# Kernel tuning notes

Measured on AMD Instinct MI355X. Metric: run time of the kernel, lower is better.

The kernel has to match this reference:

```python
import jax, jax.numpy as jnp
import numpy as np

N_QUBITS = 16
DEPTH = 4
BATCH = 512
DIM = 2 ** N_QUBITS


def _rot_matrix(tx, ty, tz):
    """Combined U = RZ(tz) @ RY(ty) @ RX(tx) per batch element. t* : [B] -> U : [B,2,2] complex64."""
    cx = jnp.cos(tx / 2).astype(jnp.complex64); sx = jnp.sin(tx / 2).astype(jnp.complex64)
    cy = jnp.cos(ty / 2).astype(jnp.complex64); sy = jnp.sin(ty / 2).astype(jnp.complex64)
    ez = jnp.exp(-1j * (tz / 2).astype(jnp.complex64))
    RX = jnp.stack([jnp.stack([cx, -1j * sx], -1), jnp.stack([-1j * sx, cx], -1)], -2)
    RY = jnp.stack([jnp.stack([cy, -sy], -1), jnp.stack([sy, cy], -1)], -2)
    zr = jnp.zeros_like(ez)
    RZ = jnp.stack([jnp.stack([ez, zr], -1), jnp.stack([zr, jnp.conj(ez)], -1)], -2)
    return jnp.einsum('bij,bjk,bkl->bil', RZ, RY, RX)


def _apply_1q(state, U, q):
    """Apply per-sample 2x2 gate U [B,2,2] on wire q (wire 0 = most significant bit)."""
    B = state.shape[0]
    st = state.reshape(B, 2 ** q, 2, 2 ** (N_QUBITS - 1 - q))
    st = jnp.einsum('bij,bajc->baic', U, st)
    return st.reshape(B, DIM)


def _apply_cnot(state, c, t):
    """CNOT with control wire c, target wire t."""
    B = state.shape[0]
    st = state.reshape((B,) + (2,) * N_QUBITS)
    ctrl0 = jax.lax.index_in_dim(st, 0, axis=1 + c, keepdims=True)
    ctrl1 = jnp.flip(jax.lax.index_in_dim(st, 1, axis=1 + c, keepdims=True), axis=1 + t)
    st = jnp.concatenate([ctrl0, ctrl1], axis=1 + c)
    return st.reshape(B, DIM)


def setup_inputs() -> dict:
    key = jax.random.key(0)
    k1, k2 = jax.random.split(key)
    x = jax.random.normal(k1, (BATCH, N_QUBITS), dtype=jnp.float32)
    params = jax.random.normal(k2, (DEPTH, N_QUBITS, 3), dtype=jnp.float32)
    return {"x": x, "params": params}


def reference(x, params):
    angles = jnp.tanh(x)  # [B, n_qubits]
    B = angles.shape[0]
    state = jnp.zeros((B, DIM), dtype=jnp.complex64).at[:, 0].set(1.0)
    for d in range(DEPTH):
        for q in range(N_QUBITS):
            a = angles[:, q]
            U = _rot_matrix(a + params[d, q, 0], a + params[d, q, 1], a + params[d, q, 2])
            state = _apply_1q(state, U, q)
        for q in range(N_QUBITS - 1):
            state = _apply_cnot(state, q, q + 1)
        state = _apply_cnot(N_QUBITS - 1 and state or state, N_QUBITS - 1, 0) if False else _apply_cnot(state, N_QUBITS - 1, 0)
    probs = (state.real ** 2 + state.imag ** 2)  # [B, DIM]
    zs = []
    for q in range(N_QUBITS):
        p = probs.reshape(B, 2 ** q, 2, 2 ** (N_QUBITS - 1 - q))
        zs.append((p[:, :, 0, :] - p[:, :, 1, :]).sum(axis=(1, 2)))
    return jnp.stack(zs, axis=1)  # [B, n_qubits]
```

## Files before the change

### kernel.cpp

```cpp
#include <hip/hip_runtime.h>
#include <cstdint>
#include <utility>

#define NQ 16
#define NDEPTH 4
#define NBATCH 512
#define NTHR 512
#define NAMP 128
#define NREG 93
#define NLDS (NAMP - NREG)

typedef float vf2 __attribute__((ext_vector_type(2)));
typedef float vf4 __attribute__((ext_vector_type(4)));

struct Masks {
  unsigned short delta[NDEPTH][NQ];
  unsigned short rowm[NDEPTH][NQ];
  unsigned short meas[NQ];
};

constexpr Masks make_masks() {
  Masks m = {};
  unsigned short Arow[NQ] = {};
  unsigned short Ainv[NQ] = {};
  for (int p = 0; p < NQ; ++p) {
    Arow[p] = (unsigned short)(1u << p);
    Ainv[p] = (unsigned short)(1u << p);
  }
  for (int d = 0; d < NDEPTH; ++d) {
    for (int q = 0; q < NQ; ++q) {
      m.delta[d][q] = Ainv[15 - q];
      m.rowm[d][q]  = Arow[15 - q];
    }
    for (int q = 0; q < NQ - 1; ++q) {
      const int pc = 15 - q, pt = 15 - (q + 1);
      Arow[pt] = (unsigned short)(Arow[pt] ^ Arow[pc]);
      Ainv[pc] = (unsigned short)(Ainv[pc] ^ Ainv[pt]);
    }
    {
      const int pc = 0, pt = 15;
      Arow[pt] = (unsigned short)(Arow[pt] ^ Arow[pc]);
      Ainv[pc] = (unsigned short)(Ainv[pc] ^ Ainv[pt]);
    }
  }
  for (int q = 0; q < NQ; ++q) m.meas[q] = Arow[15 - q];
  return m;
}

constexpr Masks MK = make_masks();

constexpr int cpar(int v) {
  int p = 0;
  for (int i = 0; i < 16; ++i) p ^= (v >> i) & 1;
  return p;
}

template<typename F, int... Is>
__device__ __forceinline__ void sf_impl(F&& f, std::integer_sequence<int, Is...>) {
  (f(std::integral_constant<int, Is>{}), ...);
}
template<int N, typename F>
__device__ __forceinline__ void static_for(F&& f) {
  sf_impl(f, std::make_integer_sequence<int, N>{});
}

__device__ __forceinline__ vf2 swap2(vf2 v) {
  return __builtin_shufflevector(v, v, 1, 0);
}
__device__ __forceinline__ vf2 upd(vf2 Arr, vf2 Ain, vf2 Brr, vf2 Bin,
                                   vf2 m, vf2 p) {
  vf2 t = Arr * m;
  t = __builtin_elementwise_fma(Ain, swap2(m), t);
  t = __builtin_elementwise_fma(Brr, p, t);
  t = __builtin_elementwise_fma(Bin, swap2(p), t);
  return t;
}

template<int r>
__device__ __forceinline__ vf2 getamp(const vf2 (&s)[NREG], const vf2* sst, int tid) {
  if constexpr (r < NREG) return s[r];
  else return sst[(r - NREG) * NTHR + tid];
}
template<int r>
__device__ __forceinline__ void putamp(vf2 (&s)[NREG], vf2* sst, int tid, vf2 v) {
  if constexpr (r < NREG) s[r] = v;
  else sst[(r - NREG) * NTHR + tid] = v;
}

template<int D, int Q>
__device__ __forceinline__ void apply_gate(vf2 (&s)[NREG], vf2* sst, vf4* xch,
                                           const vf4* utab, int tid) {
  constexpr int DLT   = MK.delta[D][Q];
  constexpr int R     = MK.rowm[D][Q];
  constexpr int dreg  = DLT & (NAMP - 1);
  constexpr int dthr  = DLT >> 7;
  constexpr int dlane = dthr & 63;
  constexpr int dwave = dthr >> 6;

  const int pt = __popc(tid & (R >> 7)) & 1;
  const int gbase = (D * NQ + Q) * 4;
  const int o0 = pt << 1;
  const int o1 = 2 - o0;
  const vf4 ca0 = utab[gbase + o0], cb0 = utab[gbase + o0 + 1];
  const vf4 ca1 = utab[gbase + o1], cb1 = utab[gbase + o1 + 1];
  const vf2 A0rr = {ca0.x, ca0.y}, A0in = {ca0.z, ca0.w};
  const vf2 B0rr = {cb0.x, cb0.y}, B0in = {cb0.z, cb0.w};
  const vf2 A1rr = {ca1.x, ca1.y}, A1in = {ca1.z, ca1.w};
  const vf2 B1rr = {cb1.x, cb1.y}, B1in = {cb1.z, cb1.w};

  if constexpr (dthr == 0) {
    static_for<NAMP>([&](auto rc) {
      constexpr int r = decltype(rc)::value;
      constexpr int r2 = r ^ dreg;
      if constexpr (r < r2) {
        constexpr int p0 = cpar(r & R);
        constexpr int p1 = cpar(r2 & R);
        const vf2 a = getamp<r >(s, sst, tid);
        const vf2 c = getamp<r2>(s, sst, tid);
        const vf2 n0 = p0 ? upd(A1rr, A1in, B1rr, B1in, a, c)
                           : upd(A0rr, A0in, B0rr, B0in, a, c);
        const vf2 n1 = p1 ? upd(A1rr, A1in, B1rr, B1in, c, a)
                           : upd(A0rr, A0in, B0rr, B0in, c, a);
        putamp<r >(s, sst, tid, n0);
        putamp<r2>(s, sst, tid, n1);
      }
    });
  } else if constexpr (dwave == 0) {
    if constexpr (dreg == 0) {
      static_for<4>([&](auto bc) {
        constexpr int BB = decltype(bc)::value;
        static_for<32>([&](auto jc) {
          constexpr int r = 32 * BB + decltype(jc)::value;
          constexpr int p0 = cpar(r & R);
          const vf2 m = getamp<r>(s, sst, tid);
          vf2 p;
          p.x = __shfl_xor(m.x, dlane);
          p.y = __shfl_xor(m.y, dlane);
          const vf2 n = p0 ? upd(A1rr, A1in, B1rr, B1in, m, p)
                            : upd(A0rr, A0in, B0rr, B0in, m, p);
          putamp<r>(s, sst, tid, n);
        });
        __builtin_amdgcn_sched_barrier(0);
      });
    } else {
      static_for<4>([&](auto bc) {
        constexpr int BB = decltype(bc)::value;
        static_for<32>([&](auto jc) {
          constexpr int r = 32 * BB + decltype(jc)::value;
          constexpr int r2 = r ^ dreg;
          if constexpr (r < r2) {
            constexpr int p0 = cpar(r & R);
            constexpr int p1 = cpar(r2 & R);
            const vf2 m0 = getamp<r >(s, sst, tid);
            const vf2 m1 = getamp<r2>(s, sst, tid);
            vf2 p0v, p1v;
            p0v.x = __shfl_xor(m1.x, dlane);
            p0v.y = __shfl_xor(m1.y, dlane);
            p1v.x = __shfl_xor(m0.x, dlane);
            p1v.y = __shfl_xor(m0.y, dlane);
            const vf2 n0 = p0 ? upd(A1rr, A1in, B1rr, B1in, m0, p0v)
                               : upd(A0rr, A0in, B0rr, B0in, m0, p0v);
            const vf2 n1 = p1 ? upd(A1rr, A1in, B1rr, B1in, m1, p1v)
                               : upd(A0rr, A0in, B0rr, B0in, m1, p1v);
            putamp<r >(s, sst, tid, n0);
            putamp<r2>(s, sst, tid, n1);
          }
        });
        __builtin_amdgcn_sched_barrier(0);
      });
    }
  } else {
    const int ptid = tid ^ dthr;
    if constexpr (dreg < 4) {
      static_for<NAMP / 4>([&](auto kc) {
        constexpr int k = decltype(kc)::value;
        const vf2 m0 = getamp<4 * k + 0>(s, sst, tid);
        const vf2 m1 = getamp<4 * k + 1>(s, sst, tid);
        const vf2 m2 = getamp<4 * k + 2>(s, sst, tid);
        const vf2 m3 = getamp<4 * k + 3>(s, sst, tid);
        xch[tid]        = (vf4){m0.x, m0.y, m1.x, m1.y};
        xch[NTHR + tid] = (vf4){m2.x, m2.y, m3.x, m3.y};
        __syncthreads();
        const vf4 q0 = xch[ptid];
        const vf4 q1 = xch[NTHR + ptid];
        static_for<4>([&](auto jc) {
          constexpr int j = decltype(jc)::value;
          constexpr int r = 4 * k + j;
          constexpr int jp = j ^ dreg;
          constexpr int p0 = cpar(r & R);
          const vf2 m = (j == 0) ? m0 : (j == 1) ? m1 : (j == 2) ? m2 : m3;
          vf2 p;
          if constexpr (jp == 0)      p = (vf2){q0.x, q0.y};
          else if constexpr (jp == 1) p = (vf2){q0.z, q0.w};
          else if constexpr (jp == 2) p = (vf2){q1.x, q1.y};
          else                        p = (vf2){q1.z, q1.w};
          const vf2 n = p0 ? upd(A1rr, A1in, B1rr, B1in, m, p)
                            : upd(A0rr, A0in, B0rr, B0in, m, p);
          putamp<r>(s, sst, tid, n);
        });
        __syncthreads();
      });
    } else {
      constexpr int kx = dreg >> 2;
      constexpr int dj = dreg & 3;
      static_for<NAMP / 4>([&](auto cc) {
        constexpr int c = decltype(cc)::value;
        if constexpr (c < (c ^ kx)) {
          constexpr int c2 = c ^ kx;
          {
            const vf2 a0 = getamp<4 * c + 0>(s, sst, tid);
            const vf2 a1 = getamp<4 * c + 1>(s, sst, tid);
            const vf2 a2 = getamp<4 * c + 2>(s, sst, tid);
            const vf2 a3 = getamp<4 * c + 3>(s, sst, tid);
            xch[tid]        = (vf4){a0.x, a0.y, a1.x, a1.y};
            xch[NTHR + tid] = (vf4){a2.x, a2.y, a3.x, a3.y};
          }
          __syncthreads();
          vf2 t0, t1, t2, t3;
          {
            const vf4 q0 = xch[ptid];
            const vf4 q1 = xch[NTHR + ptid];
            static_for<4>([&](auto jc) {
              constexpr int j = decltype(jc)::value;
              constexpr int r = 4 * c2 + j;
              constexpr int jp = j ^ dj;
              constexpr int p0 = cpar(r & R);
              const vf2 m = getamp<r>(s, sst, tid);
              vf2 p;
              if constexpr (jp == 0)      p = (vf2){q0.x, q0.y};
              else if constexpr (jp == 1) p = (vf2){q0.z, q0.w};
              else if constexpr (jp == 2) p = (vf2){q1.x, q1.y};
              else                        p = (vf2){q1.z, q1.w};
              const vf2 n = p0 ? upd(A1rr, A1in, B1rr, B1in, m, p)
                                : upd(A0rr, A0in, B0rr, B0in, m, p);
              if constexpr (j == 0) t0 = n;
              else if constexpr (j == 1) t1 = n;
              else if constexpr (j == 2) t2 = n;
              else t3 = n;
            });
          }
          __syncthreads();
          {
            const vf2 a0 = getamp<4 * c2 + 0>(s, sst, tid);
            const vf2 a1 = getamp<4 * c2 + 1>(s, sst, tid);
            const vf2 a2 = getamp<4 * c2 + 2>(s, sst, tid);
            const vf2 a3 = getamp<4 * c2 + 3>(s, sst, tid);
            xch[tid]        = (vf4){a0.x, a0.y, a1.x, a1.y};
            xch[NTHR + tid] = (vf4){a2.x, a2.y, a3.x, a3.y};
          }
          __syncthreads();
          {
            const vf4 q0 = xch[ptid];
            const vf4 q1 = xch[NTHR + ptid];
            static_for<4>([&](auto jc) {
              constexpr int j = decltype(jc)::value;
              constexpr int r = 4 * c + j;
              constexpr int jp = j ^ dj;
              constexpr int p0 = cpar(r & R);
              const vf2 m = getamp<r>(s, sst, tid);
              vf2 p;
              if constexpr (jp == 0)      p = (vf2){q0.x, q0.y};
              else if constexpr (jp == 1) p = (vf2){q0.z, q0.w};
              else if constexpr (jp == 2) p = (vf2){q1.x, q1.y};
              else                        p = (vf2){q1.z, q1.w};
              const vf2 n = p0 ? upd(A1rr, A1in, B1rr, B1in, m, p)
                                : upd(A0rr, A0in, B0rr, B0in, m, p);
              putamp<r>(s, sst, tid, n);
            });
          }
          putamp<4 * c2 + 0>(s, sst, tid, t0);
          putamp<4 * c2 + 1>(s, sst, tid, t1);
          putamp<4 * c2 + 2>(s, sst, tid, t2);
          putamp<4 * c2 + 3>(s, sst, tid, t3);
          __syncthreads();
        }
      });
    }
  }
}

template<int D, int Q>
__device__ __forceinline__ void apply_all(vf2 (&s)[NREG], vf2* sst, vf4* xch,
                                          const vf4* utab, int tid) {
  apply_gate<D, Q>(s, sst, xch, utab, tid);
  __builtin_amdgcn_sched_barrier(0);
  if constexpr (Q < NQ - 1) {
    apply_all<D, Q + 1>(s, sst, xch, utab, tid);
  } else if constexpr (D < NDEPTH - 1) {
    apply_all<D + 1, 0>(s, sst, xch, utab, tid);
  }
}

__global__ __launch_bounds__(NTHR)
__attribute__((amdgpu_waves_per_eu(2, 2)))
void qsim_kernel(const float* __restrict__ x,
                 const float* __restrict__ params,
                 float* __restrict__ out) {
  __shared__ vf2 sst[NLDS * NTHR];
  __shared__ vf4 xch[2 * NTHR];
  __shared__ vf4 utab[NDEPTH * NQ * 4];

  const int tid = threadIdx.x;
  const int b = blockIdx.x;

  if (tid < NDEPTH * NQ) {
    const int d = tid / NQ, q = tid % NQ;
    const float a = tanhf(x[b * NQ + q]);
    const float tx = a + params[(d * NQ + q) * 3 + 0];
    const float ty = a + params[(d * NQ + q) * 3 + 1];
    const float tz = a + params[(d * NQ + q) * 3 + 2];
    const float cx = cosf(0.5f * tx), sx = sinf(0.5f * tx);
    const float cy = cosf(0.5f * ty), sy = sinf(0.5f * ty);
    const float cz = cosf(0.5f * tz), sz = sinf(0.5f * tz);
    const float m00r = cy * cx,  m00i =  sy * sx;
    const float m01r = -sy * cx, m01i = -cy * sx;
    const float m10r = sy * cx,  m10i = -cy * sx;
    const float m11r = cy * cx,  m11i = -sy * sx;
    const float u00r = cz * m00r + sz * m00i, u00i = cz * m00i - sz * m00r;
    const float u01r = cz * m01r + sz * m01i, u01i = cz * m01i - sz * m01r;
    const float u10r = cz * m10r - sz * m10i, u10i = cz * m10i + sz * m10r;
    const float u11r = cz * m11r - sz * m11i, u11i = cz * m11i + sz * m11r;
    vf4* slot = utab + tid * 4;
    slot[0] = (vf4){u00r, u00r, -u00i, u00i};
    slot[1] = (vf4){u01r, u01r, -u01i, u01i};
    slot[2] = (vf4){u11r, u11r, -u11i, u11i};
    slot[3] = (vf4){u10r, u10r, -u10i, u10i};
  }

  vf2 s[NREG];
  static_for<NREG>([&](auto rc) { s[decltype(rc)::value] = (vf2){0.f, 0.f}; });
  static_for<NLDS>([&](auto ic) {
    sst[decltype(ic)::value * NTHR + tid] = (vf2){0.f, 0.f};
  });
  if (tid == 0) s[0].x = 1.0f;
  __syncthreads();

  apply_all<0, 0>(s, sst, xch, utab, tid);

  __syncthreads();
  float* red = (float*)xch;
  static_for<2>([&](auto hc) {
    constexpr int H = decltype(hc)::value;
    float z[8];
    static_for<8>([&](auto qc) { z[decltype(qc)::value] = 0.f; });
    static_for<NAMP>([&](auto rc) {
      constexpr int r = decltype(rc)::value;
      const vf2 v = getamp<r>(s, sst, tid);
      const float pr = v.x * v.x + v.y * v.y;
      static_for<8>([&](auto qc) {
        constexpr int qq = decltype(qc)::value;
        constexpr int q = 8 * H + qq;
        constexpr bool neg = cpar(r & MK.meas[q]) != 0;
        z[qq] = neg ? (z[qq] - pr) : (z[qq] + pr);
      });
    });
    static_for<8>([&](auto qc) {
      constexpr int qq = decltype(qc)::value;
      constexpr int q = 8 * H + qq;
      const int ptq = __popc(tid & (MK.meas[q] >> 7)) & 1;
      float v = ptq ? -z[qq] : z[qq];
      static_for<6>([&](auto ic) {
        constexpr int sh = 32 >> decltype(ic)::value;
        v += __shfl_xor(v, sh);
      });
      z[qq] = v;
    });
    if ((tid & 63) == 0) {
      const int w = tid >> 6;
      static_for<8>([&](auto qc) {
        constexpr int qq = decltype(qc)::value;
        red[w * 8 + qq] = z[qq];
      });
    }
    __syncthreads();
    if (tid < 8) {
      float acc = 0.f;
#pragma unroll
      for (int w = 0; w < 8; ++w) acc += red[w * 8 + tid];
      out[b * NQ + 8 * H + tid] = acc;
    }
    __syncthreads();
  });
}

extern "C" void kernel_launch(void* const* d_in, const int* in_sizes, int n_in,
                              void* d_out, int out_size, void* d_ws, size_t ws_size,
                              hipStream_t stream) {
  const float* x      = (const float*)d_in[0];
  const float* params = (const float*)d_in[1];
  float* out          = (float*)d_out;
  qsim_kernel<<<dim3(NBATCH), dim3(NTHR), 0, stream>>>(x, params, out);
}
```

Measured before the change: 854.3 us.

## Use DPP for small lane swaps and halve barriers in cross-wave gate exchange

Cross-lane exchanges with XOR distances 1, 2, 3, 7 and 15 now use DPP update instructions instead of ds_bpermute-based shuffles. The cross-wave exchange path is unified: each round stages two 4-amplitude groups (8 amplitudes) through a larger LDS buffer and uses one barrier pair per 8 amplitudes, instead of two or four barriers per group. The register-resident amplitude count rises from 93 to 97 to cut LDS-resident state. Risks include register pressure or spills at the fixed two waves per EU, and the doubled exchange buffer raising LDS use.

```diff
diff --git a/kernel.cpp b/kernel.cpp
--- a/kernel.cpp
+++ b/kernel.cpp
@@ -7,7 +7,7 @@
 #define NBATCH 512
 #define NTHR 512
 #define NAMP 128
-#define NREG 93
+#define NREG 97
 #define NLDS (NAMP - NREG)
 
 typedef float vf2 __attribute__((ext_vector_type(2)));
@@ -55,6 +55,11 @@
   return p;
 }
 
+constexpr int dppctrl(int dl) {
+  return dl == 1 ? 0xB1 : dl == 2 ? 0x4E : dl == 3 ? 0x1B
+       : dl == 7 ? 0x141 : dl == 15 ? 0x140 : -1;
+}
+
 template<typename F, int... Is>
 __device__ __forceinline__ void sf_impl(F&& f, std::integer_sequence<int, Is...>) {
   (f(std::integral_constant<int, Is>{}), ...);
@@ -76,6 +81,22 @@
   return t;
 }
 
+template<int DL>
+__device__ __forceinline__ vf2 xlane(vf2 v) {
+  constexpr int C = dppctrl(DL);
+  if constexpr (C >= 0) {
+    int xi = __float_as_int(v.x), yi = __float_as_int(v.y);
+    xi = __builtin_amdgcn_update_dpp(xi, xi, C, 0xF, 0xF, true);
+    yi = __builtin_amdgcn_update_dpp(yi, yi, C, 0xF, 0xF, true);
+    return (vf2){__int_as_float(xi), __int_as_float(yi)};
+  } else {
+    vf2 p;
+    p.x = __shfl_xor(v.x, DL);
+    p.y = __shfl_xor(v.y, DL);
+    return p;
+  }
+}
+
 template<int r>
 __device__ __forceinline__ vf2 getamp(const vf2 (&s)[NREG], const vf2* sst, int tid) {
   if constexpr (r < NREG) return s[r];
@@ -85,6 +106,12 @@
 __device__ __forceinline__ void putamp(vf2 (&s)[NREG], vf2* sst, int tid, vf2 v) {
   if constexpr (r < NREG) s[r] = v;
   else sst[(r - NREG) * NTHR + tid] = v;
+}
+template<int r>
+__device__ __forceinline__ vf4 pack2(const vf2 (&s)[NREG], const vf2* sst, int tid) {
+  const vf2 a = getamp<r    >(s, sst, tid);
+  const vf2 b = getamp<r + 1>(s, sst, tid);
+  return (vf4){a.x, a.y, b.x, b.y};
 }
 
 template<int D, int Q>
@@ -133,9 +160,7 @@
           constexpr int r = 32 * BB + decltype(jc)::value;
           constexpr int p0 = cpar(r & R);
           const vf2 m = getamp<r>(s, sst, tid);
-          vf2 p;
-          p.x = __shfl_xor(m.x, dlane);
-          p.y = __shfl_xor(m.y, dlane);
+          const vf2 p = xlane<dlane>(m);
           const vf2 n = p0 ? upd(A1rr, A1in, B1rr, B1in, m, p)
                             : upd(A0rr, A0in, B0rr, B0in, m, p);
           putamp<r>(s, sst, tid, n);
@@ -153,11 +178,8 @@
             constexpr int p1 = cpar(r2 & R);
             const vf2 m0 = getamp<r >(s, sst, tid);
             const vf2 m1 = getamp<r2>(s, sst, tid);
-            vf2 p0v, p1v;
-            p0v.x = __shfl_xor(m1.x, dlane);
-            p0v.y = __shfl_xor(m1.y, dlane);
-            p1v.x = __shfl_xor(m0.x, dlane);
-            p1v.y = __shfl_xor(m0.y, dlane);
+            const vf2 p0v = xlane<dlane>(m1);
+            const vf2 p1v = xlane<dlane>(m0);
             const vf2 n0 = p0 ? upd(A1rr, A1in, B1rr, B1in, m0, p0v)
                                : upd(A0rr, A0in, B0rr, B0in, m0, p0v);
             const vf2 n1 = p1 ? upd(A1rr, A1in, B1rr, B1in, m1, p1v)
@@ -170,112 +192,43 @@
       });
     }
   } else {
+    constexpr int kc0 = dreg >> 2;
+    constexpr int kc  = kc0 ? kc0 : 1;
     const int ptid = tid ^ dthr;
-    if constexpr (dreg < 4) {
-      static_for<NAMP / 4>([&](auto kc) {
-        constexpr int k = decltype(kc)::value;
-        const vf2 m0 = getamp<4 * k + 0>(s, sst, tid);
-        const vf2 m1 = getamp<4 * k + 1>(s, sst, tid);
-        const vf2 m2 = getamp<4 * k + 2>(s, sst, tid);
-        const vf2 m3 = getamp<4 * k + 3>(s, sst, tid);
-        xch[tid]        = (vf4){m0.x, m0.y, m1.x, m1.y};
-        xch[NTHR + tid] = (vf4){m2.x, m2.y, m3.x, m3.y};
+    static_for<NAMP / 4>([&](auto cc) {
+      constexpr int c = decltype(cc)::value;
+      if constexpr (c < (c ^ kc)) {
+        constexpr int c2 = c ^ kc;
+        xch[0 * NTHR + tid] = pack2<4 * c  + 0>(s, sst, tid);
+        xch[1 * NTHR + tid] = pack2<4 * c  + 2>(s, sst, tid);
+        xch[2 * NTHR + tid] = pack2<4 * c2 + 0>(s, sst, tid);
+        xch[3 * NTHR + tid] = pack2<4 * c2 + 2>(s, sst, tid);
         __syncthreads();
-        const vf4 q0 = xch[ptid];
-        const vf4 q1 = xch[NTHR + ptid];
-        static_for<4>([&](auto jc) {
-          constexpr int j = decltype(jc)::value;
-          constexpr int r = 4 * k + j;
-          constexpr int jp = j ^ dreg;
+        const vf4 q0 = xch[0 * NTHR + ptid];
+        const vf4 q1 = xch[1 * NTHR + ptid];
+        const vf4 q2 = xch[2 * NTHR + ptid];
+        const vf4 q3 = xch[3 * NTHR + ptid];
+        static_for<8>([&](auto jc) {
+          constexpr int jj = decltype(jc)::value;
+          constexpr int r  = (jj < 4) ? (4 * c + jj) : (4 * c2 + (jj - 4));
+          constexpr int rp = r ^ dreg;
+          constexpr int sb = ((rp >> 2) == c) ? 0 : 2;
+          constexpr int slot = sb + ((rp & 3) >> 1);
+          constexpr int half = rp & 1;
           constexpr int p0 = cpar(r & R);
-          const vf2 m = (j == 0) ? m0 : (j == 1) ? m1 : (j == 2) ? m2 : m3;
           vf2 p;
-          if constexpr (jp == 0)      p = (vf2){q0.x, q0.y};
-          else if constexpr (jp == 1) p = (vf2){q0.z, q0.w};
-          else if constexpr (jp == 2) p = (vf2){q1.x, q1.y};
-          else                        p = (vf2){q1.z, q1.w};
+          if constexpr (slot == 0)      p = half ? (vf2){q0.z, q0.w} : (vf2){q0.x, q0.y};
+          else if constexpr (slot == 1) p = half ? (vf2){q1.z, q1.w} : (vf2){q1.x, q1.y};
+          else if constexpr (slot == 2) p = half ? (vf2){q2.z, q2.w} : (vf2){q2.x, q2.y};
+          else                          p = half ? (vf2){q3.z, q3.w} : (vf2){q3.x, q3.y};
+          const vf2 m = getamp<r>(s, sst, tid);
           const vf2 n = p0 ? upd(A1rr, A1in, B1rr, B1in, m, p)
                             : upd(A0rr, A0in, B0rr, B0in, m, p);
           putamp<r>(s, sst, tid, n);
         });
         __syncthreads();
-      });
-    } else {
-      constexpr int kx = dreg >> 2;
-      constexpr int dj = dreg & 3;
-      static_for<NAMP / 4>([&](auto cc) {
-        constexpr int c = decltype(cc)::value;
-        if constexpr (c < (c ^ kx)) {
-          constexpr int c2 = c ^ kx;
-          {
-            const vf2 a0 = getamp<4 * c + 0>(s, sst, tid);
-            const vf2 a1 = getamp<4 * c + 1>(s, sst, tid);
-            const vf2 a2 = getamp<4 * c + 2>(s, sst, tid);
-            const vf2 a3 = getamp<4 * c + 3>(s, sst, tid);
-            xch[tid]        = (vf4){a0.x, a0.y, a1.x, a1.y};
-            xch[NTHR + tid] = (vf4){a2.x, a2.y, a3.x, a3.y};
-          }
-          __syncthreads();
-          vf2 t0, t1, t2, t3;
-          {
-            const vf4 q0 = xch[ptid];
-            const vf4 q1 = xch[NTHR + ptid];
-            static_for<4>([&](auto jc) {
-              constexpr int j = decltype(jc)::value;
-              constexpr int r = 4 * c2 + j;
-              constexpr int jp = j ^ dj;
-              constexpr int p0 = cpar(r & R);
-              const vf2 m = getamp<r>(s, sst, tid);
-              vf2 p;
-              if constexpr (jp == 0)      p = (vf2){q0.x, q0.y};
-              else if constexpr (jp == 1) p = (vf2){q0.z, q0.w};
-              else if constexpr (jp == 2) p = (vf2){q1.x, q1.y};
-              else                        p = (vf2){q1.z, q1.w};
-              const vf2 n = p0 ? upd(A1rr, A1in, B1rr, B1in, m, p)
-                                : upd(A0rr, A0in, B0rr, B0in, m, p);
-              if constexpr (j == 0) t0 = n;
-              else if constexpr (j == 1) t1 = n;
-              else if constexpr (j == 2) t2 = n;
-              else t3 = n;
-            });
-          }
-          __syncthreads();
-          {
-            const vf2 a0 = getamp<4 * c2 + 0>(s, sst, tid);
-            const vf2 a1 = getamp<4 * c2 + 1>(s, sst, tid);
-            const vf2 a2 = getamp<4 * c2 + 2>(s, sst, tid);
-            const vf2 a3 = getamp<4 * c2 + 3>(s, sst, tid);
-            xch[tid]        = (vf4){a0.x, a0.y, a1.x, a1.y};
-            xch[NTHR + tid] = (vf4){a2.x, a2.y, a3.x, a3.y};
-          }
-          __syncthreads();
-          {
-            const vf4 q0 = xch[ptid];
-            const vf4 q1 = xch[NTHR + ptid];
-            static_for<4>([&](auto jc) {
-              constexpr int j = decltype(jc)::value;
-              constexpr int r = 4 * c + j;
-              constexpr int jp = j ^ dj;
-              constexpr int p0 = cpar(r & R);
-              const vf2 m = getamp<r>(s, sst, tid);
-              vf2 p;
-              if constexpr (jp == 0)      p = (vf2){q0.x, q0.y};
-              else if constexpr (jp == 1) p = (vf2){q0.z, q0.w};
-              else if constexpr (jp == 2) p = (vf2){q1.x, q1.y};
-              else                        p = (vf2){q1.z, q1.w};
-              const vf2 n = p0 ? upd(A1rr, A1in, B1rr, B1in, m, p)
-                                : upd(A0rr, A0in, B0rr, B0in, m, p);
-              putamp<r>(s, sst, tid, n);
-            });
-          }
-          putamp<4 * c2 + 0>(s, sst, tid, t0);
-          putamp<4 * c2 + 1>(s, sst, tid, t1);
-          putamp<4 * c2 + 2>(s, sst, tid, t2);
-          putamp<4 * c2 + 3>(s, sst, tid, t3);
-          __syncthreads();
-        }
-      });
-    }
+      }
+    });
   }
 }
 
@@ -297,7 +250,7 @@
                  const float* __restrict__ params,
                  float* __restrict__ out) {
   __shared__ vf2 sst[NLDS * NTHR];
-  __shared__ vf4 xch[2 * NTHR];
+  __shared__ vf4 xch[4 * NTHR];
   __shared__ vf4 utab[NDEPTH * NQ * 4];
 
   const int tid = threadIdx.x;
```

Result: faster. 769.8 us (-9.9%).
